# Optimization experiments

Hardware: AMD Instinct MI355X
Metric: run time of the kernel (lower is better)

Reference implementation:

```python
import jax, jax.numpy as jnp
import numpy as np

HIDDEN = 1024
HEADS = 16
HEAD_DIM = HIDDEN // HEADS


def setup_inputs() -> dict:
    key = jax.random.key(0)
    ks = jax.random.split(key, 11)
    B, N, D = 2, 2048, HIDDEN
    scale = 1.0 / np.sqrt(D)
    inp = {
        "q": jax.random.normal(ks[0], (B, N, D), jnp.float32),
        "k": jax.random.normal(ks[1], (B, N, D), jnp.float32),
        "v": jax.random.normal(ks[2], (B, N, D), jnp.float32),
        "Wq": jax.random.normal(ks[3], (D, D), jnp.float32) * scale,
        "bq": jnp.zeros((D,), jnp.float32),
        "Wk": jax.random.normal(ks[4], (D, D), jnp.float32) * scale,
        "bk": jnp.zeros((D,), jnp.float32),
        "Wv": jax.random.normal(ks[5], (D, D), jnp.float32) * scale,
        "bv": jnp.zeros((D,), jnp.float32),
        "Wo": jax.random.normal(ks[6], (D, D), jnp.float32) * scale,
        "bo": jnp.zeros((D,), jnp.float32),
    }
    return inp


def _split_heads(x):  # [b, n, h*d] -> [b, h, n, d]
    b, n, _ = x.shape
    return x.reshape(b, n, HEADS, HEAD_DIM).transpose(0, 2, 1, 3)


def reference(q, k, v, Wq, bq, Wk, bk, Wv, bv, Wo, bo):
    # Linear projections (torch Linear: x @ W.T + b)
    Q = _split_heads(q @ Wq.T + bq)   # [b, h, n, d]
    K = _split_heads(k @ Wk.T + bk)   # [b, h, n, d]
    V = _split_heads(v @ Wv.T + bv)   # [b, h, n, d]
    scale = 1.0 / jnp.sqrt(jnp.asarray(HEAD_DIM, Q.dtype))
    scores = jnp.einsum("bhnd,bhmd->bhnm", Q, K) * scale  # [b, h, n, n]
    attn = jax.nn.softmax(scores, axis=-1)
    out = jnp.einsum("bhnm,bhmd->bhnd", attn, V)          # [b, h, n, d]
    b, h, n, d = out.shape
    out = out.transpose(0, 2, 1, 3).reshape(b, n, h * d)  # [b, n, h*d]
    return out @ Wo.T + bo
```

## Files before the change

kernel.cpp:

```cpp
#include <hip/hip_runtime.h>
#include <hip/hip_bf16.h>
#include <cstdint>
#include <cstddef>

#define DDIM 1024
#define NHEADS 16
#define HDIM 64
#define NSEQ 2048
#define NTOK 4096
#define QSCALE 0.18033688011112042f

typedef float f32x4 __attribute__((ext_vector_type(4)));
typedef float f32x16 __attribute__((ext_vector_type(16)));
typedef __bf16 bf16x8 __attribute__((ext_vector_type(8)));
typedef unsigned short u16x8 __attribute__((ext_vector_type(8)));

typedef __attribute__((address_space(1))) const unsigned int gq_t;
typedef __attribute__((address_space(3))) unsigned int lq_t;

__device__ __forceinline__ unsigned short f2bf(float f) {
    union { float f; unsigned int u; } v; v.f = f;
    unsigned int u = v.u;
    u += 0x7FFFu + ((u >> 16) & 1u);
    return (unsigned short)(u >> 16);
}

__device__ __forceinline__ float exp2_fast(float x) {
    float r;
    asm("v_exp_f32 %0, %1\n\ts_nop 0" : "=v"(r) : "v"(x));
    return r;
}

__device__ __forceinline__ unsigned cvtpk_bf16(float lo, float hi) {
    unsigned r;
    asm("v_cvt_pk_bf16_f32 %0, %1, %2" : "=v"(r) : "v"(lo), "v"(hi));
    return r;
}

#define PSWAP(a, b) asm("v_permlane32_swap_b32 %0, %1" : "+v"(a), "+v"(b))

__global__ __launch_bounds__(256) void cvt3_kernel(
    const float* __restrict__ a0, const float* __restrict__ a1,
    const float* __restrict__ a2, unsigned short* __restrict__ d0,
    unsigned short* __restrict__ d1, unsigned short* __restrict__ d2) {
    int z = blockIdx.z;
    const float* s = z == 0 ? a0 : z == 1 ? a1 : a2;
    unsigned short* d = z == 0 ? d0 : z == 1 ? d1 : d2;
    int i = blockIdx.x * 256 + threadIdx.x;
    const float4* s4 = (const float4*)s + (size_t)i * 2;
    float4 a = s4[0], b = s4[1];
    unsigned short o[8] __attribute__((aligned(16)));
    o[0] = f2bf(a.x); o[1] = f2bf(a.y); o[2] = f2bf(a.z); o[3] = f2bf(a.w);
    o[4] = f2bf(b.x); o[5] = f2bf(b.y); o[6] = f2bf(b.z); o[7] = f2bf(b.w);
    *(u16x8*)(d + (size_t)i * 8) = *(const u16x8*)o;
}

__global__ __launch_bounds__(256) void cvt4_kernel(
    const float* __restrict__ a0, const float* __restrict__ a1,
    const float* __restrict__ a2, const float* __restrict__ a3,
    unsigned short* __restrict__ d0, unsigned short* __restrict__ d1,
    unsigned short* __restrict__ d2, unsigned short* __restrict__ d3) {
    int z = blockIdx.z;
    const float* s = z == 0 ? a0 : z == 1 ? a1 : z == 2 ? a2 : a3;
    unsigned short* d = z == 0 ? d0 : z == 1 ? d1 : z == 2 ? d2 : d3;
    int i = blockIdx.x * 256 + threadIdx.x;
    const float4* s4 = (const float4*)s + (size_t)i * 2;
    float4 a = s4[0], b = s4[1];
    unsigned short o[8] __attribute__((aligned(16)));
    o[0] = f2bf(a.x); o[1] = f2bf(a.y); o[2] = f2bf(a.z); o[3] = f2bf(a.w);
    o[4] = f2bf(b.x); o[5] = f2bf(b.y); o[6] = f2bf(b.z); o[7] = f2bf(b.w);
    *(u16x8*)(d + (size_t)i * 8) = *(const u16x8*)o;
}

__device__ __forceinline__ void gemm_body(const unsigned short* __restrict__ A,
                                          const unsigned short* __restrict__ W,
                                          const float* __restrict__ bias,
                                          int mode, void* __restrict__ Cout) {
    __shared__ __align__(16) unsigned short As[128 * 32];
    __shared__ __align__(16) unsigned short Bs[128 * 32];
    const int tid = threadIdx.x, lane = tid & 63, wid = tid >> 6;
    const int r = lane & 15, g = lane >> 4;
    const int mbase = blockIdx.y * 128;
    const int nbase = blockIdx.x * 128;
    const int wm = (wid >> 1) * 64, wn = (wid & 1) * 64;

    f32x4 zero = {0.f, 0.f, 0.f, 0.f};
    f32x4 acc[4][4];
#pragma unroll
    for (int mi = 0; mi < 4; ++mi)
#pragma unroll
        for (int ni = 0; ni < 4; ++ni) acc[mi][ni] = zero;

    for (int kt = 0; kt < 1024; kt += 32) {
        __syncthreads();
#pragma unroll
        for (int j = 0; j < 2; ++j) {
            int ub = wid * 64 + j * 256;
            int uu = ub + lane;
            const unsigned short* ga =
                A + (size_t)(mbase + (uu >> 2)) * 1024 + kt + (uu & 3) * 8;
            __builtin_amdgcn_global_load_lds((gq_t*)ga, (lq_t*)(As + ub * 8), 16, 0, 0);
            const unsigned short* gb =
                W + (size_t)(nbase + (uu >> 2)) * 1024 + kt + (uu & 3) * 8;
            __builtin_amdgcn_global_load_lds((gq_t*)gb, (lq_t*)(Bs + ub * 8), 16, 0, 0);
        }
        __syncthreads();
        bf16x8 af[4], bf[4];
#pragma unroll
        for (int mi = 0; mi < 4; ++mi)
            af[mi] = *(const bf16x8*)(As + (wm + mi * 16 + r) * 32 + g * 8);
#pragma unroll
        for (int ni = 0; ni < 4; ++ni)
            bf[ni] = *(const bf16x8*)(Bs + (wn + ni * 16 + r) * 32 + g * 8);
#pragma unroll
        for (int mi = 0; mi < 4; ++mi)
#pragma unroll
            for (int ni = 0; ni < 4; ++ni)
                acc[mi][ni] = __builtin_amdgcn_mfma_f32_16x16x32_bf16(
                    af[mi], bf[ni], acc[mi][ni], 0, 0, 0);
    }
#pragma unroll
    for (int mi = 0; mi < 4; ++mi) {
#pragma unroll
        for (int ni = 0; ni < 4; ++ni) {
            int c = nbase + wn + ni * 16 + r;
            float bv = bias[c];
#pragma unroll
            for (int rr = 0; rr < 4; ++rr) {
                int m = mbase + wm + mi * 16 + g * 4 + rr;
                float val = acc[mi][ni][rr] + bv;
                if (mode == 0) {
                    ((unsigned short*)Cout)[(size_t)m * 1024 + c] = f2bf(val * QSCALE);
                } else if (mode == 1) {
                    size_t addr = ((size_t)((m >> 11) * 16 + (c >> 6)) * 2048 +
                                   (size_t)(m & 2047)) * 64 + (c & 63);
                    ((unsigned short*)Cout)[addr] = f2bf(val);
                } else if (mode == 2) {
                    ((unsigned short*)Cout)[(size_t)m * 1024 + c] = f2bf(val);
                } else {
                    ((float*)Cout)[(size_t)m * 1024 + c] = val;
                }
            }
        }
    }
}

__global__ __launch_bounds__(256) void gemm_qkv_kernel(
    const unsigned short* __restrict__ qb, const unsigned short* __restrict__ kb,
    const unsigned short* __restrict__ vb, const unsigned short* __restrict__ Wq,
    const unsigned short* __restrict__ Wk, const unsigned short* __restrict__ Wv,
    const float* __restrict__ bq, const float* __restrict__ bk,
    const float* __restrict__ bv, unsigned short* __restrict__ Qp,
    unsigned short* __restrict__ Kp, unsigned short* __restrict__ Vp) {
    int z = blockIdx.z;
    const unsigned short* A = (z == 0) ? qb : (z == 1) ? kb : vb;
    const unsigned short* W = (z == 0) ? Wq : (z == 1) ? Wk : Wv;
    const float* bias = (z == 0) ? bq : (z == 1) ? bk : bv;
    unsigned short* C = (z == 0) ? Qp : (z == 1) ? Kp : Vp;
    gemm_body(A, W, bias, z, C);
}

__global__ __launch_bounds__(256) void gemm_out_kernel(
    const unsigned short* __restrict__ AO, const unsigned short* __restrict__ Wo,
    const float* __restrict__ bo, float* __restrict__ out) {
    gemm_body(AO, Wo, bo, 3, out);
}

__global__ __launch_bounds__(256) void vtrans_kernel(
    const unsigned short* __restrict__ Vp, unsigned short* __restrict__ Vt) {
    __shared__ __align__(16) unsigned short T[64 * 80];
    const int tid = threadIdx.x;
    const int n0 = blockIdx.x * 64, bh = blockIdx.y;
    const int b = bh >> 4, h = bh & 15;
    const unsigned short* src = Vp + (size_t)(b * NSEQ + n0) * DDIM + h * HDIM;
#pragma unroll
    for (int j = 0; j < 2; ++j) {
        int idx = j * 256 + tid;
        int n = idx >> 3, c = (idx & 7) * 8;
        u16x8 val = *(const u16x8*)(src + (size_t)n * DDIM + c);
        *(u16x8*)(&T[n * 80 + c]) = val;
    }
    __syncthreads();
    unsigned short* dst = Vt + (size_t)bh * HDIM * NSEQ + n0;
#pragma unroll
    for (int j = 0; j < 2; ++j) {
        int idx = j * 256 + tid;
        int d = idx >> 3, nn = (idx & 7) * 8, rot = idx & 7;
        unsigned short o[8] __attribute__((aligned(16)));
#pragma unroll
        for (int e0 = 0; e0 < 8; ++e0) {
            int e = (e0 + rot) & 7;
            o[e] = T[(nn + e) * 80 + d];
        }
        *(u16x8*)(dst + (size_t)d * NSEQ + nn) = *(const u16x8*)o;
    }
}

__global__ __launch_bounds__(256, 2) void attn_kernel(
    const unsigned short* __restrict__ Qp,
    const unsigned short* __restrict__ Kh,
    const unsigned short* __restrict__ Vt,
    unsigned short* __restrict__ AO) {
    __shared__ __align__(16) unsigned short Ks[2][4096];
    __shared__ __align__(16) unsigned short Vs[2][4096];

    const int tid = threadIdx.x, lane = tid & 63, wid = tid >> 6;
    const int q31 = lane & 31, hi = lane >> 5;

    int bid = blockIdx.x;
    int swz = (bid & 7) * 64 + (bid >> 3);
    const int bh = swz >> 4, b = bh >> 4, h = bh & 15;
    const int qbase = ((swz & 15) * 4 + wid) * 32;

    const unsigned short* Kt = Kh + (size_t)bh * (NSEQ * HDIM);
    const unsigned short* Vb = Vt + (size_t)bh * (HDIM * NSEQ);

    bf16x8 qf[4];
    {
        const unsigned short* qp =
            Qp + (size_t)(b * NSEQ + qbase + q31) * DDIM + h * HDIM + hi * 8;
#pragma unroll
        for (int t = 0; t < 4; ++t) qf[t] = *(const bf16x8*)(qp + t * 16);
    }

    const size_t koff0 = (size_t)q31 * HDIM + (wid & 3) * 16 + hi * 8;
    const size_t koff1 = koff0 + 32 * HDIM;
    const size_t voff0 =
        (size_t)q31 * NSEQ + ((wid >> 1) & 1) * 32 + (wid & 1) * 16 + hi * 8;
    const size_t voff1 = voff0 + (size_t)32 * NSEQ;
    const int lb0 = wid * 512, lb1 = wid * 512 + 2048;

    auto STAGE = [&](int buf, int kv0) {
        const unsigned short* kbase = Kt + (size_t)kv0 * HDIM;
        __builtin_amdgcn_global_load_lds((gq_t*)(kbase + koff0),
                                         (lq_t*)(&Ks[buf][lb0]), 16, 0, 0);
        __builtin_amdgcn_global_load_lds((gq_t*)(kbase + koff1),
                                         (lq_t*)(&Ks[buf][lb1]), 16, 0, 0);
        const unsigned short* vbase = Vb + kv0;
        __builtin_amdgcn_global_load_lds((gq_t*)(vbase + voff0),
                                         (lq_t*)(&Vs[buf][lb0]), 16, 0, 0);
        __builtin_amdgcn_global_load_lds((gq_t*)(vbase + voff1),
                                         (lq_t*)(&Vs[buf][lb1]), 16, 0, 0);
    };

    f32x16 oA0, oB0, oA1, oB1;
#pragma unroll
    for (int i = 0; i < 16; ++i) {
        oA0[i] = 0.f; oB0[i] = 0.f; oA1[i] = 0.f; oB1[i] = 0.f;
    }
    float m0 = -3.0e38f, l0 = 0.f, m1 = -3.0e38f, l1 = 0.f;

    union PB { unsigned u[4]; bf16x8 v; };

    auto QK = [&](int cur, int s) -> f32x16 {
        const unsigned short* kf = &Ks[cur][s * 2048 + lane * 8];
        f32x16 st;
#pragma unroll
        for (int i = 0; i < 16; ++i) st[i] = 0.f;
#pragma unroll
        for (int t = 0; t < 4; ++t)
            st = __builtin_amdgcn_mfma_f32_32x32x16_bf16(
                *(const bf16x8*)(kf + t * 512), qf[t], st, 0, 0, 0);
        return st;
    };

    auto SM = [&](const f32x16& st, float& m, float& l, f32x16& oA, f32x16& oB,
                  PB& P0, PB& P1) {
        float m8[8], m4[4];
#pragma unroll
        for (int j = 0; j < 8; ++j) m8[j] = fmaxf(st[2 * j], st[2 * j + 1]);
#pragma unroll
        for (int j = 0; j < 4; ++j) m4[j] = fmaxf(m8[2 * j], m8[2 * j + 1]);
        float pm = fmaxf(fmaxf(m4[0], m4[1]), fmaxf(m4[2], m4[3]));
        pm = fmaxf(pm, __shfl_xor(pm, 32, 64));

        if (__any(pm - m > 8.0f)) {
            float mn = fmaxf(m, pm);
            float al = exp2_fast(m - mn);
            m = mn;
            l *= al;
#pragma unroll
            for (int i = 0; i < 16; ++i) { oA[i] *= al; oB[i] *= al; }
        }

        float p[16];
#pragma unroll
        for (int i = 0; i < 16; ++i) p[i] = exp2_fast(st[i] - m);
        float s8[8], s4[4];
#pragma unroll
        for (int j = 0; j < 8; ++j) s8[j] = p[2 * j] + p[2 * j + 1];
#pragma unroll
        for (int j = 0; j < 4; ++j) s4[j] = s8[2 * j] + s8[2 * j + 1];
        float rs = (s4[0] + s4[1]) + (s4[2] + s4[3]);
        rs += __shfl_xor(rs, 32, 64);
        l += rs;

        unsigned w0 = cvtpk_bf16(p[0], p[1]), w1 = cvtpk_bf16(p[2], p[3]);
        unsigned w2 = cvtpk_bf16(p[4], p[5]), w3 = cvtpk_bf16(p[6], p[7]);
        unsigned w4 = cvtpk_bf16(p[8], p[9]), w5 = cvtpk_bf16(p[10], p[11]);
        unsigned w6 = cvtpk_bf16(p[12], p[13]), w7 = cvtpk_bf16(p[14], p[15]);
        PSWAP(w0, w2); PSWAP(w1, w3); PSWAP(w4, w6); PSWAP(w5, w7);
        P0.u[0] = w0; P0.u[1] = w1; P0.u[2] = w2; P0.u[3] = w3;
        P1.u[0] = w4; P1.u[1] = w5; P1.u[2] = w6; P1.u[3] = w7;
    };

    auto PV = [&](int cur, int s, const PB& P0, const PB& P1, f32x16& oA,
                  f32x16& oB) {
        const unsigned short* vf0 = &Vs[cur][s * 1024 + lane * 8];
        const unsigned short* vf1 = &Vs[cur][2048 + s * 1024 + lane * 8];
        oA = __builtin_amdgcn_mfma_f32_32x32x16_bf16(
            *(const bf16x8*)(vf0), P0.v, oA, 0, 0, 0);
        oA = __builtin_amdgcn_mfma_f32_32x32x16_bf16(
            *(const bf16x8*)(vf0 + 512), P1.v, oA, 0, 0, 0);
        oB = __builtin_amdgcn_mfma_f32_32x32x16_bf16(
            *(const bf16x8*)(vf1), P0.v, oB, 0, 0, 0);
        oB = __builtin_amdgcn_mfma_f32_32x32x16_bf16(
            *(const bf16x8*)(vf1 + 512), P1.v, oB, 0, 0, 0);
    };

    STAGE(0, 0);
    int cur = 0;
    for (int it = 0; it < 32; ++it) {
        STAGE(cur ^ 1, ((it + 1) & 31) * 64);
        asm volatile("s_waitcnt vmcnt(4)" ::: "memory");
        __builtin_amdgcn_s_barrier();
        __builtin_amdgcn_sched_barrier(0);
        __builtin_amdgcn_s_setprio(1);
        f32x16 st0 = QK(cur, 0);
        f32x16 st1 = QK(cur, 1);
        __builtin_amdgcn_s_setprio(0);
        PB P00, P01, P10, P11;
        SM(st0, m0, l0, oA0, oB0, P00, P01);
        SM(st1, m1, l1, oA1, oB1, P10, P11);
        __builtin_amdgcn_s_setprio(1);
        PV(cur, 0, P00, P01, oA0, oB0);
        PV(cur, 1, P10, P11, oA1, oB1);
        __builtin_amdgcn_s_setprio(0);
        __builtin_amdgcn_sched_barrier(0);
        asm volatile("" ::: "memory");
        __builtin_amdgcn_s_barrier();
        cur ^= 1;
    }

    float mt = fmaxf(m0, m1);
    float a0 = exp2_fast(m0 - mt), a1 = exp2_fast(m1 - mt);
    float inv = 1.0f / (l0 * a0 + l1 * a1);
    unsigned short* op = AO + (size_t)(b * NSEQ + qbase + q31) * DDIM + h * HDIM;
#pragma unroll
    for (int r2 = 0; r2 < 16; ++r2) {
        int d = (r2 & 3) + 8 * (r2 >> 2) + 4 * hi;
        op[d] = f2bf((oA0[r2] * a0 + oA1[r2] * a1) * inv);
        op[d + 32] = f2bf((oB0[r2] * a0 + oB1[r2] * a1) * inv);
    }
}

extern "C" void kernel_launch(void* const* d_in, const int* in_sizes, int n_in,
                              void* d_out, int out_size, void* d_ws, size_t ws_size,
                              hipStream_t stream) {
    const float* q = (const float*)d_in[0];
    const float* k = (const float*)d_in[1];
    const float* v = (const float*)d_in[2];
    const float* Wq = (const float*)d_in[3];
    const float* bq = (const float*)d_in[4];
    const float* Wk = (const float*)d_in[5];
    const float* bk = (const float*)d_in[6];
    const float* Wv = (const float*)d_in[7];
    const float* bv = (const float*)d_in[8];
    const float* Wo = (const float*)d_in[9];
    const float* bo = (const float*)d_in[10];
    float* out = (float*)d_out;

    unsigned short* ws = (unsigned short*)d_ws;
    const size_t TOKD = (size_t)NTOK * DDIM;
    const size_t WD = (size_t)DDIM * DDIM;
    unsigned short* qb = ws;
    unsigned short* kb = qb + TOKD;
    unsigned short* vb = kb + TOKD;
    unsigned short* Wqb = vb + TOKD;
    unsigned short* Wkb = Wqb + WD;
    unsigned short* Wvb = Wkb + WD;
    unsigned short* Wob = Wvb + WD;
    unsigned short* Qp = Wob + WD;
    unsigned short* Kp = Qp + TOKD;
    unsigned short* Vp = Kp + TOKD;
    unsigned short* AOp = Vp + TOKD;
    unsigned short* Vtb = qb;

    const int tok8 = (int)(TOKD / 8);
    const int w8 = (int)(WD / 8);
    cvt3_kernel<<<dim3(tok8 / 256, 1, 3), 256, 0, stream>>>(q, k, v, qb, kb, vb);
    cvt4_kernel<<<dim3(w8 / 256, 1, 4), 256, 0, stream>>>(Wq, Wk, Wv, Wo,
                                                          Wqb, Wkb, Wvb, Wob);
    gemm_qkv_kernel<<<dim3(8, 32, 3), 256, 0, stream>>>(qb, kb, vb, Wqb, Wkb, Wvb,
                                                        bq, bk, bv, Qp, Kp, Vp);
    vtrans_kernel<<<dim3(32, 32), 256, 0, stream>>>(Vp, Vtb);
    attn_kernel<<<512, 256, 0, stream>>>(Qp, Kp, Vtb, AOp);
    gemm_out_kernel<<<dim3(8, 32), 256, 0, stream>>>(AOp, Wob, bo, out);
}
```

Before: 149.9 us.

## Merge conversion kernels, double GEMM and attention K tile depth

The two fp32-to-bf16 conversion launches become one seven-slice launch, with an early exit for the smaller weight slices. The GEMM K-step goes from 32 to 64, with an MFMA-fragment-ordered LDS layout and raised wave priority around the MFMAs. The attention kernel stages 128 keys per iteration instead of 64, halving the loop trips and barriers, and processes two sub-blocks per online-softmax chain. The aim is fewer launches and fewer synchronisations per unit of work, at the cost of doubled LDS use, which may reduce occupancy.

```diff
diff --git a/kernel.cpp b/kernel.cpp
--- a/kernel.cpp
+++ b/kernel.cpp
@@ -39,14 +39,23 @@
 
 #define PSWAP(a, b) asm("v_permlane32_swap_b32 %0, %1" : "+v"(a), "+v"(b))
 
-__global__ __launch_bounds__(256) void cvt3_kernel(
+__global__ __launch_bounds__(256) void cvt_all_kernel(
     const float* __restrict__ a0, const float* __restrict__ a1,
-    const float* __restrict__ a2, unsigned short* __restrict__ d0,
-    unsigned short* __restrict__ d1, unsigned short* __restrict__ d2) {
+    const float* __restrict__ a2, const float* __restrict__ a3,
+    const float* __restrict__ a4, const float* __restrict__ a5,
+    const float* __restrict__ a6, unsigned short* __restrict__ d0,
+    unsigned short* __restrict__ d1, unsigned short* __restrict__ d2,
+    unsigned short* __restrict__ d3, unsigned short* __restrict__ d4,
+    unsigned short* __restrict__ d5, unsigned short* __restrict__ d6,
+    int tok8, int w8) {
     int z = blockIdx.z;
-    const float* s = z == 0 ? a0 : z == 1 ? a1 : a2;
-    unsigned short* d = z == 0 ? d0 : z == 1 ? d1 : d2;
+    const float* s = z == 0 ? a0 : z == 1 ? a1 : z == 2 ? a2 : z == 3 ? a3
+                     : z == 4 ? a4 : z == 5 ? a5 : a6;
+    unsigned short* d = z == 0 ? d0 : z == 1 ? d1 : z == 2 ? d2 : z == 3 ? d3
+                        : z == 4 ? d4 : z == 5 ? d5 : d6;
+    int n8 = (z < 3) ? tok8 : w8;
     int i = blockIdx.x * 256 + threadIdx.x;
+    if (i >= n8) return;
     const float4* s4 = (const float4*)s + (size_t)i * 2;
     float4 a = s4[0], b = s4[1];
     unsigned short o[8] __attribute__((aligned(16)));
@@ -55,29 +64,12 @@
     *(u16x8*)(d + (size_t)i * 8) = *(const u16x8*)o;
 }
 
-__global__ __launch_bounds__(256) void cvt4_kernel(
-    const float* __restrict__ a0, const float* __restrict__ a1,
-    const float* __restrict__ a2, const float* __restrict__ a3,
-    unsigned short* __restrict__ d0, unsigned short* __restrict__ d1,
-    unsigned short* __restrict__ d2, unsigned short* __restrict__ d3) {
-    int z = blockIdx.z;
-    const float* s = z == 0 ? a0 : z == 1 ? a1 : z == 2 ? a2 : a3;
-    unsigned short* d = z == 0 ? d0 : z == 1 ? d1 : z == 2 ? d2 : d3;
-    int i = blockIdx.x * 256 + threadIdx.x;
-    const float4* s4 = (const float4*)s + (size_t)i * 2;
-    float4 a = s4[0], b = s4[1];
-    unsigned short o[8] __attribute__((aligned(16)));
-    o[0] = f2bf(a.x); o[1] = f2bf(a.y); o[2] = f2bf(a.z); o[3] = f2bf(a.w);
-    o[4] = f2bf(b.x); o[5] = f2bf(b.y); o[6] = f2bf(b.z); o[7] = f2bf(b.w);
-    *(u16x8*)(d + (size_t)i * 8) = *(const u16x8*)o;
-}
-
 __device__ __forceinline__ void gemm_body(const unsigned short* __restrict__ A,
                                           const unsigned short* __restrict__ W,
                                           const float* __restrict__ bias,
                                           int mode, void* __restrict__ Cout) {
-    __shared__ __align__(16) unsigned short As[128 * 32];
-    __shared__ __align__(16) unsigned short Bs[128 * 32];
+    __shared__ __align__(16) unsigned short As[8192];
+    __shared__ __align__(16) unsigned short Bs[8192];
     const int tid = threadIdx.x, lane = tid & 63, wid = tid >> 6;
     const int r = lane & 15, g = lane >> 4;
     const int mbase = blockIdx.y * 128;
@@ -91,33 +83,41 @@
 #pragma unroll
         for (int ni = 0; ni < 4; ++ni) acc[mi][ni] = zero;
 
-    for (int kt = 0; kt < 1024; kt += 32) {
+    for (int kt = 0; kt < 1024; kt += 64) {
         __syncthreads();
 #pragma unroll
-        for (int j = 0; j < 2; ++j) {
-            int ub = wid * 64 + j * 256;
-            int uu = ub + lane;
+        for (int j = 0; j < 4; ++j) {
+            int blk = j * 4 + wid;
+            int t = blk >> 1, kk = blk & 1;
             const unsigned short* ga =
-                A + (size_t)(mbase + (uu >> 2)) * 1024 + kt + (uu & 3) * 8;
-            __builtin_amdgcn_global_load_lds((gq_t*)ga, (lq_t*)(As + ub * 8), 16, 0, 0);
+                A + (size_t)(mbase + t * 16 + r) * 1024 + kt + kk * 32 + g * 8;
+            __builtin_amdgcn_global_load_lds((gq_t*)ga, (lq_t*)(As + blk * 512),
+                                             16, 0, 0);
             const unsigned short* gb =
-                W + (size_t)(nbase + (uu >> 2)) * 1024 + kt + (uu & 3) * 8;
-            __builtin_amdgcn_global_load_lds((gq_t*)gb, (lq_t*)(Bs + ub * 8), 16, 0, 0);
+                W + (size_t)(nbase + t * 16 + r) * 1024 + kt + kk * 32 + g * 8;
+            __builtin_amdgcn_global_load_lds((gq_t*)gb, (lq_t*)(Bs + blk * 512),
+                                             16, 0, 0);
         }
         __syncthreads();
-        bf16x8 af[4], bf[4];
-#pragma unroll
-        for (int mi = 0; mi < 4; ++mi)
-            af[mi] = *(const bf16x8*)(As + (wm + mi * 16 + r) * 32 + g * 8);
-#pragma unroll
-        for (int ni = 0; ni < 4; ++ni)
-            bf[ni] = *(const bf16x8*)(Bs + (wn + ni * 16 + r) * 32 + g * 8);
-#pragma unroll
-        for (int mi = 0; mi < 4; ++mi)
+        const int ta = (wid >> 1) * 4, tb = (wid & 1) * 4;
+#pragma unroll
+        for (int kk = 0; kk < 2; ++kk) {
+            bf16x8 af[4], bf[4];
+#pragma unroll
+            for (int mi = 0; mi < 4; ++mi)
+                af[mi] = *(const bf16x8*)(As + ((ta + mi) * 2 + kk) * 512 + lane * 8);
 #pragma unroll
             for (int ni = 0; ni < 4; ++ni)
-                acc[mi][ni] = __builtin_amdgcn_mfma_f32_16x16x32_bf16(
-                    af[mi], bf[ni], acc[mi][ni], 0, 0, 0);
+                bf[ni] = *(const bf16x8*)(Bs + ((tb + ni) * 2 + kk) * 512 + lane * 8);
+            __builtin_amdgcn_s_setprio(1);
+#pragma unroll
+            for (int mi = 0; mi < 4; ++mi)
+#pragma unroll
+                for (int ni = 0; ni < 4; ++ni)
+                    acc[mi][ni] = __builtin_amdgcn_mfma_f32_16x16x32_bf16(
+                        af[mi], bf[ni], acc[mi][ni], 0, 0, 0);
+            __builtin_amdgcn_s_setprio(0);
+        }
     }
 #pragma unroll
     for (int mi = 0; mi < 4; ++mi) {
@@ -201,8 +201,8 @@
     const unsigned short* __restrict__ Kh,
     const unsigned short* __restrict__ Vt,
     unsigned short* __restrict__ AO) {
-    __shared__ __align__(16) unsigned short Ks[2][4096];
-    __shared__ __align__(16) unsigned short Vs[2][4096];
+    __shared__ __align__(16) unsigned short Ks[2][8192];
+    __shared__ __align__(16) unsigned short Vs[2][8192];
 
     const int tid = threadIdx.x, lane = tid & 63, wid = tid >> 6;
     const int q31 = lane & 31, hi = lane >> 5;
@@ -223,24 +223,26 @@
         for (int t = 0; t < 4; ++t) qf[t] = *(const bf16x8*)(qp + t * 16);
     }
 
-    const size_t koff0 = (size_t)q31 * HDIM + (wid & 3) * 16 + hi * 8;
-    const size_t koff1 = koff0 + 32 * HDIM;
-    const size_t voff0 =
-        (size_t)q31 * NSEQ + ((wid >> 1) & 1) * 32 + (wid & 1) * 16 + hi * 8;
-    const size_t voff1 = voff0 + (size_t)32 * NSEQ;
-    const int lb0 = wid * 512, lb1 = wid * 512 + 2048;
+    const size_t kro = (size_t)q31 * HDIM + wid * 16 + hi * 8;
+    const size_t vro = (size_t)q31 * NSEQ + hi * 8;
 
     auto STAGE = [&](int buf, int kv0) {
-        const unsigned short* kbase = Kt + (size_t)kv0 * HDIM;
-        __builtin_amdgcn_global_load_lds((gq_t*)(kbase + koff0),
-                                         (lq_t*)(&Ks[buf][lb0]), 16, 0, 0);
-        __builtin_amdgcn_global_load_lds((gq_t*)(kbase + koff1),
-                                         (lq_t*)(&Ks[buf][lb1]), 16, 0, 0);
-        const unsigned short* vbase = Vb + kv0;
-        __builtin_amdgcn_global_load_lds((gq_t*)(vbase + voff0),
-                                         (lq_t*)(&Vs[buf][lb0]), 16, 0, 0);
-        __builtin_amdgcn_global_load_lds((gq_t*)(vbase + voff1),
-                                         (lq_t*)(&Vs[buf][lb1]), 16, 0, 0);
+#pragma unroll
+        for (int j = 0; j < 4; ++j) {
+            const unsigned short* gk =
+                Kt + (size_t)(kv0 + j * 32) * HDIM + kro;
+            __builtin_amdgcn_global_load_lds(
+                (gq_t*)gk, (lq_t*)(&Ks[buf][j * 2048 + wid * 512]), 16, 0, 0);
+        }
+#pragma unroll
+        for (int j = 0; j < 4; ++j) {
+            int blk = j * 4 + wid;
+            int dh = blk >> 3, ks = blk & 7;
+            const unsigned short* gv =
+                Vb + (size_t)(dh * 32) * NSEQ + vro + kv0 + ks * 16;
+            __builtin_amdgcn_global_load_lds(
+                (gq_t*)gv, (lq_t*)(&Vs[buf][blk * 512]), 16, 0, 0);
+        }
     };
 
     f32x16 oA0, oB0, oA1, oB1;
@@ -268,9 +270,9 @@
                   PB& P0, PB& P1) {
         float m8[8], m4[4];
 #pragma unroll
-        for (int j = 0; j < 8; ++j) m8[j] = fmaxf(st[2 * j], st[2 * j + 1]);
-#pragma unroll
-        for (int j = 0; j < 4; ++j) m4[j] = fmaxf(m8[2 * j], m8[2 * j + 1]);
+        for (int j2 = 0; j2 < 8; ++j2) m8[j2] = fmaxf(st[2 * j2], st[2 * j2 + 1]);
+#pragma unroll
+        for (int j2 = 0; j2 < 4; ++j2) m4[j2] = fmaxf(m8[2 * j2], m8[2 * j2 + 1]);
         float pm = fmaxf(fmaxf(m4[0], m4[1]), fmaxf(m4[2], m4[3]));
         pm = fmaxf(pm, __shfl_xor(pm, 32, 64));
 
@@ -288,9 +290,9 @@
         for (int i = 0; i < 16; ++i) p[i] = exp2_fast(st[i] - m);
         float s8[8], s4[4];
 #pragma unroll
-        for (int j = 0; j < 8; ++j) s8[j] = p[2 * j] + p[2 * j + 1];
-#pragma unroll
-        for (int j = 0; j < 4; ++j) s4[j] = s8[2 * j] + s8[2 * j + 1];
+        for (int j2 = 0; j2 < 8; ++j2) s8[j2] = p[2 * j2] + p[2 * j2 + 1];
+#pragma unroll
+        for (int j2 = 0; j2 < 4; ++j2) s4[j2] = s8[2 * j2] + s8[2 * j2 + 1];
         float rs = (s4[0] + s4[1]) + (s4[2] + s4[3]);
         rs += __shfl_xor(rs, 32, 64);
         l += rs;
@@ -306,8 +308,8 @@
 
     auto PV = [&](int cur, int s, const PB& P0, const PB& P1, f32x16& oA,
                   f32x16& oB) {
-        const unsigned short* vf0 = &Vs[cur][s * 1024 + lane * 8];
-        const unsigned short* vf1 = &Vs[cur][2048 + s * 1024 + lane * 8];
+        const unsigned short* vf0 = &Vs[cur][(s * 2) * 512 + lane * 8];
+        const unsigned short* vf1 = vf0 + 4096;
         oA = __builtin_amdgcn_mfma_f32_32x32x16_bf16(
             *(const bf16x8*)(vf0), P0.v, oA, 0, 0, 0);
         oA = __builtin_amdgcn_mfma_f32_32x32x16_bf16(
@@ -320,21 +322,32 @@
 
     STAGE(0, 0);
     int cur = 0;
-    for (int it = 0; it < 32; ++it) {
-        STAGE(cur ^ 1, ((it + 1) & 31) * 64);
-        asm volatile("s_waitcnt vmcnt(4)" ::: "memory");
+    for (int it = 0; it < 16; ++it) {
+        STAGE(cur ^ 1, ((it + 1) & 15) * 128);
+        asm volatile("s_waitcnt vmcnt(8)" ::: "memory");
         __builtin_amdgcn_s_barrier();
         __builtin_amdgcn_sched_barrier(0);
         __builtin_amdgcn_s_setprio(1);
-        f32x16 st0 = QK(cur, 0);
-        f32x16 st1 = QK(cur, 1);
+        f32x16 stA = QK(cur, 0);
+        f32x16 stB = QK(cur, 2);
         __builtin_amdgcn_s_setprio(0);
         PB P00, P01, P10, P11;
-        SM(st0, m0, l0, oA0, oB0, P00, P01);
-        SM(st1, m1, l1, oA1, oB1, P10, P11);
+        SM(stA, m0, l0, oA0, oB0, P00, P01);
+        SM(stB, m1, l1, oA1, oB1, P10, P11);
         __builtin_amdgcn_s_setprio(1);
         PV(cur, 0, P00, P01, oA0, oB0);
-        PV(cur, 1, P10, P11, oA1, oB1);
+        PV(cur, 2, P10, P11, oA1, oB1);
+        __builtin_amdgcn_s_setprio(0);
+        __builtin_amdgcn_s_setprio(1);
+        f32x16 stC = QK(cur, 1);
+        f32x16 stD = QK(cur, 3);
+        __builtin_amdgcn_s_setprio(0);
+        PB P20, P21, P30, P31;
+        SM(stC, m0, l0, oA0, oB0, P20, P21);
+        SM(stD, m1, l1, oA1, oB1, P30, P31);
+        __builtin_amdgcn_s_setprio(1);
+        PV(cur, 1, P20, P21, oA0, oB0);
+        PV(cur, 3, P30, P31, oA1, oB1);
         __builtin_amdgcn_s_setprio(0);
         __builtin_amdgcn_sched_barrier(0);
         asm volatile("" ::: "memory");
@@ -388,9 +401,8 @@
 
     const int tok8 = (int)(TOKD / 8);
     const int w8 = (int)(WD / 8);
-    cvt3_kernel<<<dim3(tok8 / 256, 1, 3), 256, 0, stream>>>(q, k, v, qb, kb, vb);
-    cvt4_kernel<<<dim3(w8 / 256, 1, 4), 256, 0, stream>>>(Wq, Wk, Wv, Wo,
-                                                          Wqb, Wkb, Wvb, Wob);
+    cvt_all_kernel<<<dim3(tok8 / 256, 1, 7), 256, 0, stream>>>(
+        q, k, v, Wq, Wk, Wv, Wo, qb, kb, vb, Wqb, Wkb, Wvb, Wob, tok8, w8);
     gemm_qkv_kernel<<<dim3(8, 32, 3), 256, 0, stream>>>(qb, kb, vb, Wqb, Wkb, Wvb,
                                                         bq, bk, bv, Qp, Kp, Vp);
     vtrans_kernel<<<dim3(32, 32), 256, 0, stream>>>(Vp, Vtb);
```

Result: slower. 174.0 us (+16.0%).
